# Kernel optimization log

Hardware: AMD Instinct MI355X
Metric: run time of the kernel (lower is better)

Reference implementation:

```python
import jax, jax.numpy as jnp
import numpy as np

B, L, C = 4, 2048, 512
H, D = 8, 512          # n_head, hidden_dim (per-head dim)
TEMP = 1.0
EPS = 1e-5


def setup_inputs() -> dict:
    key = jax.random.key(0)
    ks = jax.random.split(key, 12)
    s_in = 1.0 / np.sqrt(C)
    s_out = 1.0 / np.sqrt(H * D)
    return {
        "q": jax.random.normal(ks[0], (B, L, C), jnp.float32),
        "k": jax.random.normal(ks[1], (B, L, C), jnp.float32),
        "v": jax.random.normal(ks[2], (B, L, C), jnp.float32),
        "mask": jax.random.randint(ks[3], (B, L, L), 0, 2).astype(bool),
        "Wq": jax.random.normal(ks[4], (C, H * D), jnp.float32) * s_in,
        "bq": jnp.zeros((H * D,), jnp.float32),
        "Wk": jax.random.normal(ks[5], (C, H * D), jnp.float32) * s_in,
        "bk": jnp.zeros((H * D,), jnp.float32),
        "Wv": jax.random.normal(ks[6], (C, H * D), jnp.float32) * s_in,
        "bv": jnp.zeros((H * D,), jnp.float32),
        "Wo": jax.random.normal(ks[7], (H * D, D), jnp.float32) * s_out,
        "bo": jnp.zeros((D,), jnp.float32),
        "gamma": jnp.ones((D,), jnp.float32),
        "beta": jnp.zeros((D,), jnp.float32),
    }


def reference(q, k, v, mask, Wq, bq, Wk, bk, Wv, bv, Wo, bo, gamma, beta):
    b, ql, _ = q.shape
    residual = q
    qh = (q @ Wq + bq).reshape(b, ql, H, D)           # b,l,h,d
    kh = (k @ Wk + bk).reshape(b, ql, H, D)
    vh = (v @ Wv + bv).reshape(b, ql, H, D)
    # scores in head-major layout to mirror torch permute(2,0,1,3)
    scores = jnp.einsum("bqhd,bkhd->hbqk", qh, kh) / TEMP  # h,b,l,l
    scores = jnp.where(mask[None], -jnp.inf, scores)
    atten = jax.nn.softmax(scores, axis=-1)                 # h,b,l,l
    ctx = jnp.einsum("hbqk,bkhd->bqhd", atten, vh)          # b,l,h,d
    ctx = ctx.reshape(b, ql, H * D)
    out = ctx @ Wo + bo                                     # b,l,D  (dropout in eval mode)
    x = out + residual
    mu = jnp.mean(x, axis=-1, keepdims=True)
    var = jnp.var(x, axis=-1, keepdims=True)
    out = (x - mu) / jnp.sqrt(var + EPS) * gamma + beta
    return out, atten.reshape(H * b, ql, ql)
```

## Files before the change

kernel.cpp:

```cpp
#include <hip/hip_runtime.h>
#include <stdint.h>


typedef unsigned short u16;
typedef _Float16 f16;
typedef __attribute__((ext_vector_type(8))) _Float16 f16x8;
typedef __attribute__((ext_vector_type(4))) float f32x4;

#define OP_F16 0
#define OP_F32 1

#define EPI_QKH    0
#define EPI_VHT    1
#define EPI_SCORES 2
#define EPI_CTX    3
#define EPI_OUT    4

__device__ __forceinline__ f32x4 mfma16(f16x8 a, f16x8 b, f32x4 c) {
  return __builtin_amdgcn_mfma_f32_16x16x32_f16(a, b, c, 0, 0, 0);
}

__device__ __forceinline__ void stage_tile_f16(const char* gbase, size_t grow, char* lds, int tid) {
  const int lane = tid & 63, wave = tid >> 6;
#pragma unroll
  for (int c = 0; c < 2; ++c) {
    int chunk = wave * 2 + c;
    int off = chunk * 1024 + lane * 16;
    int r = off >> 6;
    int cb = off & 63;
    const char* g = gbase + (size_t)r * grow + cb;
    __builtin_amdgcn_global_load_lds(
        (__attribute__((address_space(1))) void*)g,
        (__attribute__((address_space(3))) void*)(lds + chunk * 1024),
        16, 0, 0);
  }
}

#define F32_ROWF 36
__device__ __forceinline__ void stage_tile_f32pad(const char* gbase, size_t grow, char* lds, int tid) {
#pragma unroll
  for (int c = 0; c < 4; ++c) {
    int idx = c * 256 + tid;
    int row = idx >> 3, col4 = idx & 7;
    f32x4 v = *(const f32x4*)(gbase + (size_t)row * grow + col4 * 16);
    *(f32x4*)(lds + (size_t)row * (F32_ROWF * 4) + col4 * 16) = v;
  }
}

template<int M>
__device__ __forceinline__ f16x8 load_frag(const char* lds, int row, int kq) {
  if constexpr (M == OP_F16) {
    return *(const f16x8*)(lds + ((size_t)row * 32 + kq) * 2);
  } else {
    size_t off = ((size_t)row * F32_ROWF + kq) * 4;
    f32x4 x0 = *(const f32x4*)(lds + off);
    f32x4 x1 = *(const f32x4*)(lds + off + 16);
    f16x8 h;
#pragma unroll
    for (int j = 0; j < 4; ++j) {
      h[j]     = (_Float16)x0[j];
      h[j + 4] = (_Float16)x1[j];
    }
    return h;
  }
}

template<int AM, int BM, int EPI>
__global__ __launch_bounds__(256, 2)
void gemm_k(const char* __restrict__ A, const char* __restrict__ B,
            int lda, int ldb, int K,
            char* __restrict__ C0,
            const float* __restrict__ bias, const float* __restrict__ resid) {
  constexpr int ASZ = (AM == OP_F16) ? 8192 : 128 * F32_ROWF * 4;
  constexpr int BSZ = (BM == OP_F16) ? 8192 : 128 * F32_ROWF * 4;
  __shared__ alignas(16) char smem[ASZ + BSZ];
  char* sA = smem;
  char* sB = smem + ASZ;

  const int tid = threadIdx.x, lane = tid & 63, wave = tid >> 6;
  const int wm = wave >> 1, wn = wave & 1;
  const int m0 = blockIdx.x * 128, n0 = blockIdx.y * 128;

  const char* pA = A; const char* pB = B;
  if constexpr (EPI == EPI_SCORES) {
    int z = blockIdx.z, h = z >> 2, b = z & 3;
    size_t e2 = ((size_t)b * 2048 * 4096 + (size_t)h * 512) * 2;
    pA += e2; pB += e2;
  } else if constexpr (EPI == EPI_CTX) {
    int z = blockIdx.z, h = z >> 2, b = z & 3;
    pA += ((size_t)z << 22) * 4;
    pB += ((size_t)(b * 8 + h) * 512 * 2048) * 2;
  }

  f32x4 acc[4][4];
#pragma unroll
  for (int i = 0; i < 4; ++i)
#pragma unroll
    for (int j = 0; j < 4; ++j) acc[i][j] = (f32x4){0.f, 0.f, 0.f, 0.f};

  for (int k0 = 0; k0 < K; k0 += 32) {
    if constexpr (AM == OP_F16)
      stage_tile_f16(pA + ((size_t)m0 * lda + k0) * 2, (size_t)lda * 2, sA, tid);
    else
      stage_tile_f32pad(pA + ((size_t)m0 * lda + k0) * 4, (size_t)lda * 4, sA, tid);
    if constexpr (BM == OP_F16)
      stage_tile_f16(pB + ((size_t)n0 * ldb + k0) * 2, (size_t)ldb * 2, sB, tid);
    else
      stage_tile_f32pad(pB + ((size_t)n0 * ldb + k0) * 4, (size_t)ldb * 4, sB, tid);
    __syncthreads();

    const int kq = (lane >> 4) * 8, l15 = lane & 15;
    f16x8 af[4], bf[4];
#pragma unroll
    for (int mi = 0; mi < 4; ++mi)
      af[mi] = load_frag<AM>(sA, wm * 64 + mi * 16 + l15, kq);
#pragma unroll
    for (int ni = 0; ni < 4; ++ni)
      bf[ni] = load_frag<BM>(sB, wn * 64 + ni * 16 + l15, kq);

#pragma unroll
    for (int mi = 0; mi < 4; ++mi)
#pragma unroll
      for (int ni = 0; ni < 4; ++ni)
        acc[mi][ni] = mfma16(af[mi], bf[ni], acc[mi][ni]);
    __syncthreads();
  }

  const int l15 = lane & 15, quad = lane >> 4;
#pragma unroll
  for (int mi = 0; mi < 4; ++mi)
#pragma unroll
    for (int ni = 0; ni < 4; ++ni)
#pragma unroll
      for (int r = 0; r < 4; ++r) {
        int m = m0 + wm * 64 + mi * 16 + quad * 4 + r;
        int n = n0 + wn * 64 + ni * 16 + l15;
        float v = acc[mi][ni][r];
        if constexpr (EPI == EPI_QKH) {
          v += bias[n];
          ((f16*)C0)[(size_t)m * 4096 + n] = (f16)v;
        } else if constexpr (EPI == EPI_VHT) {
          v += bias[m];
          int hh = m >> 9, d = m & 511, bb = n >> 11, ll = n & 2047;
          ((f16*)C0)[(((size_t)(bb * 8 + hh) * 512 + d) << 11) + ll] = (f16)v;
        } else if constexpr (EPI == EPI_SCORES) {
          int z = blockIdx.z;
          ((float*)C0)[((size_t)z << 22) + ((size_t)m << 11) + n] = v;
        } else if constexpr (EPI == EPI_CTX) {
          int z = blockIdx.z, hh = z >> 2, bb = z & 3;
          ((f16*)C0)[((size_t)(bb * 2048 + m) << 12) + hh * 512 + n] = (f16)v;
        } else {
          v += bias[n] + resid[((size_t)m << 9) + n];
          ((float*)C0)[((size_t)m << 9) + n] = v;
        }
      }
}

__global__ __launch_bounds__(256)
void transpose_cvt_k(const float* __restrict__ in, f16* __restrict__ T,
                     int rows_in, int cols_in) {
  int idx = blockIdx.x * 256 + threadIdx.x;
  if (idx >= rows_in * cols_in) return;
  int c = idx / rows_in, r = idx - c * rows_in;
  T[idx] = (f16)in[(size_t)r * cols_in + c];
}

__global__ __launch_bounds__(256)
void maskprep_k(const int* __restrict__ m32, unsigned char* __restrict__ m8) {
  int i = blockIdx.x * 256 + threadIdx.x;
  int4 v = ((const int4*)m32)[i];
  uchar4 c;
  c.x = (unsigned char)v.x; c.y = (unsigned char)v.y;
  c.z = (unsigned char)v.z; c.w = (unsigned char)v.w;
  ((uchar4*)m8)[i] = c;
}

__global__ __launch_bounds__(256)
void softmax_k(float* __restrict__ att, const unsigned char* __restrict__ m8) {
  __shared__ float sm[4];
  int t = threadIdx.x, lane = t & 63, wave = t >> 6;
  size_t r = blockIdx.x;
  int z = (int)(r >> 11), m = (int)(r & 2047), b = z & 3;
  float4* row = (float4*)(att + (r << 11));
  const uchar4* mrow = (const uchar4*)(m8 + (((size_t)b << 22) + ((size_t)m << 11)));
  float4 a = row[t], c = row[t + 256];
  uchar4 ma = mrow[t], mc = mrow[t + 256];
  if (ma.x) a.x = -1e30f; if (ma.y) a.y = -1e30f;
  if (ma.z) a.z = -1e30f; if (ma.w) a.w = -1e30f;
  if (mc.x) c.x = -1e30f; if (mc.y) c.y = -1e30f;
  if (mc.z) c.z = -1e30f; if (mc.w) c.w = -1e30f;
  float mx = fmaxf(fmaxf(fmaxf(a.x, a.y), fmaxf(a.z, a.w)),
                   fmaxf(fmaxf(c.x, c.y), fmaxf(c.z, c.w)));
#pragma unroll
  for (int o = 32; o > 0; o >>= 1) mx = fmaxf(mx, __shfl_xor(mx, o));
  if (lane == 0) sm[wave] = mx;
  __syncthreads();
  mx = fmaxf(fmaxf(sm[0], sm[1]), fmaxf(sm[2], sm[3]));
  a.x = __expf(a.x - mx); a.y = __expf(a.y - mx);
  a.z = __expf(a.z - mx); a.w = __expf(a.w - mx);
  c.x = __expf(c.x - mx); c.y = __expf(c.y - mx);
  c.z = __expf(c.z - mx); c.w = __expf(c.w - mx);
  float s = a.x + a.y + a.z + a.w + c.x + c.y + c.z + c.w;
#pragma unroll
  for (int o = 32; o > 0; o >>= 1) s += __shfl_xor(s, o);
  __syncthreads();
  if (lane == 0) sm[wave] = s;
  __syncthreads();
  s = sm[0] + sm[1] + sm[2] + sm[3];
  float inv = 1.0f / s;
  a.x *= inv; a.y *= inv; a.z *= inv; a.w *= inv;
  c.x *= inv; c.y *= inv; c.z *= inv; c.w *= inv;
  row[t] = a; row[t + 256] = c;
}

__global__ __launch_bounds__(256)
void ln_k(const float* __restrict__ x, const float* __restrict__ gamma,
          const float* __restrict__ beta, float* __restrict__ out) {
  __shared__ float s1[4], s2[4];
  int t = threadIdx.x, lane = t & 63, wave = t >> 6;
  size_t base = (size_t)blockIdx.x << 9;
  float2 v = ((const float2*)(x + base))[t];
  float s = v.x + v.y;
  float q = v.x * v.x + v.y * v.y;
#pragma unroll
  for (int o = 32; o > 0; o >>= 1) { s += __shfl_xor(s, o); q += __shfl_xor(q, o); }
  if (lane == 0) { s1[wave] = s; s2[wave] = q; }
  __syncthreads();
  s = s1[0] + s1[1] + s1[2] + s1[3];
  q = s2[0] + s2[1] + s2[2] + s2[3];
  float mu = s * (1.0f / 512.0f);
  float var = q * (1.0f / 512.0f) - mu * mu;
  float rs = rsqrtf(var + 1e-5f);
  float2 g = ((const float2*)gamma)[t];
  float2 bb = ((const float2*)beta)[t];
  float2 o2;
  o2.x = (v.x - mu) * rs * g.x + bb.x;
  o2.y = (v.y - mu) * rs * g.y + bb.y;
  ((float2*)(out + base))[t] = o2;
}

extern "C" void kernel_launch(void* const* d_in, const int* in_sizes, int n_in,
                              void* d_out, int out_size, void* d_ws, size_t ws_size,
                              hipStream_t stream) {
  (void)in_sizes; (void)n_in; (void)out_size; (void)ws_size;
  const float* q     = (const float*)d_in[0];
  const float* k     = (const float*)d_in[1];
  const float* v     = (const float*)d_in[2];
  const int*   mask  = (const int*)d_in[3];
  const float* Wq    = (const float*)d_in[4];
  const float* bq    = (const float*)d_in[5];
  const float* Wk    = (const float*)d_in[6];
  const float* bk    = (const float*)d_in[7];
  const float* Wv    = (const float*)d_in[8];
  const float* bv    = (const float*)d_in[9];
  const float* Wo    = (const float*)d_in[10];
  const float* bo    = (const float*)d_in[11];
  const float* gamma = (const float*)d_in[12];
  const float* beta  = (const float*)d_in[13];

  float* out0  = (float*)d_out;
  float* atten = out0 + (size_t)4 * 2048 * 512;

  char* ws = (char*)d_ws;
  const size_t MB = 1024ull * 1024ull;
  f16* WqT  = (f16*)(ws + 0 * MB);
  f16* WkT  = (f16*)(ws + 4 * MB);
  f16* WvT  = (f16*)(ws + 8 * MB);
  f16* WoT  = (f16*)(ws + 12 * MB);
  unsigned char* mask8 = (unsigned char*)(ws + 16 * MB);
  f16* vhT  = (f16*)(ws + 32 * MB);
  f16* qh   = (f16*)(ws + 96 * MB);
  f16* kh   = (f16*)(ws + 160 * MB);
  f16* ctx  = (f16*)(ws + 224 * MB);
  float* xbuf = (float*)(ws + 96 * MB);

  transpose_cvt_k<<<8192, 256, 0, stream>>>(Wq, WqT, 512, 4096);
  transpose_cvt_k<<<8192, 256, 0, stream>>>(Wk, WkT, 512, 4096);
  transpose_cvt_k<<<8192, 256, 0, stream>>>(Wv, WvT, 512, 4096);
  transpose_cvt_k<<<8192, 256, 0, stream>>>(Wo, WoT, 4096, 512);
  maskprep_k<<<16384, 256, 0, stream>>>(mask, mask8);

  gemm_k<OP_F32, OP_F16, EPI_QKH><<<dim3(64, 32, 1), 256, 0, stream>>>(
      (const char*)q, (const char*)WqT, 512, 512, 512, (char*)qh, bq, nullptr);
  gemm_k<OP_F32, OP_F16, EPI_QKH><<<dim3(64, 32, 1), 256, 0, stream>>>(
      (const char*)k, (const char*)WkT, 512, 512, 512, (char*)kh, bk, nullptr);

  gemm_k<OP_F16, OP_F32, EPI_VHT><<<dim3(32, 64, 1), 256, 0, stream>>>(
      (const char*)WvT, (const char*)v, 512, 512, 512, (char*)vhT, bv, nullptr);

  gemm_k<OP_F16, OP_F16, EPI_SCORES><<<dim3(16, 16, 32), 256, 0, stream>>>(
      (const char*)qh, (const char*)kh, 4096, 4096, 512, (char*)atten, nullptr, nullptr);

  softmax_k<<<65536, 256, 0, stream>>>(atten, mask8);

  gemm_k<OP_F32, OP_F16, EPI_CTX><<<dim3(16, 4, 32), 256, 0, stream>>>(
      (const char*)atten, (const char*)vhT, 2048, 2048, 2048, (char*)ctx, nullptr, nullptr);

  gemm_k<OP_F16, OP_F16, EPI_OUT><<<dim3(64, 4, 1), 256, 0, stream>>>(
      (const char*)ctx, (const char*)WoT, 4096, 4096, 4096, (char*)xbuf, bo, q);

  ln_k<<<8192, 256, 0, stream>>>(xbuf, gamma, beta, out0);
}
```

Baseline: 1.642 ms.

## Pre-convert GEMM operands to f16 so every GEMM uses async LDS staging

Adds a float-to-f16 conversion pass for q, k and v. Softmax now also writes an f16 copy of the attention matrix. The GEMM kernel keeps only the f16 path with direct global-to-LDS loads, which removes the register-staged padded f32 tiles and the per-fragment conversion in the inner loop. The context GEMM reads a half-size attention matrix, at the cost of an extra 256 MB write in softmax and three small conversion kernels. Workspace buffers are remapped so the f16 attention copy aliases buffers that are dead by the time softmax runs.

```diff
diff --git a/kernel.cpp b/kernel.cpp
--- a/kernel.cpp
+++ b/kernel.cpp
@@ -4,11 +4,9 @@
 
 typedef unsigned short u16;
 typedef _Float16 f16;
+typedef __attribute__((ext_vector_type(4))) _Float16 f16x4;
 typedef __attribute__((ext_vector_type(8))) _Float16 f16x8;
 typedef __attribute__((ext_vector_type(4))) float f32x4;
-
-#define OP_F16 0
-#define OP_F32 1
 
 #define EPI_QKH    0
 #define EPI_VHT    1
@@ -36,46 +34,19 @@
   }
 }
 
-#define F32_ROWF 36
-__device__ __forceinline__ void stage_tile_f32pad(const char* gbase, size_t grow, char* lds, int tid) {
-#pragma unroll
-  for (int c = 0; c < 4; ++c) {
-    int idx = c * 256 + tid;
-    int row = idx >> 3, col4 = idx & 7;
-    f32x4 v = *(const f32x4*)(gbase + (size_t)row * grow + col4 * 16);
-    *(f32x4*)(lds + (size_t)row * (F32_ROWF * 4) + col4 * 16) = v;
-  }
-}
-
-template<int M>
-__device__ __forceinline__ f16x8 load_frag(const char* lds, int row, int kq) {
-  if constexpr (M == OP_F16) {
-    return *(const f16x8*)(lds + ((size_t)row * 32 + kq) * 2);
-  } else {
-    size_t off = ((size_t)row * F32_ROWF + kq) * 4;
-    f32x4 x0 = *(const f32x4*)(lds + off);
-    f32x4 x1 = *(const f32x4*)(lds + off + 16);
-    f16x8 h;
-#pragma unroll
-    for (int j = 0; j < 4; ++j) {
-      h[j]     = (_Float16)x0[j];
-      h[j + 4] = (_Float16)x1[j];
-    }
-    return h;
-  }
-}
-
-template<int AM, int BM, int EPI>
+__device__ __forceinline__ f16x8 load_frag16(const char* lds, int row, int kq) {
+  return *(const f16x8*)(lds + ((size_t)row * 32 + kq) * 2);
+}
+
+template<int EPI>
 __global__ __launch_bounds__(256, 2)
 void gemm_k(const char* __restrict__ A, const char* __restrict__ B,
             int lda, int ldb, int K,
             char* __restrict__ C0,
             const float* __restrict__ bias, const float* __restrict__ resid) {
-  constexpr int ASZ = (AM == OP_F16) ? 8192 : 128 * F32_ROWF * 4;
-  constexpr int BSZ = (BM == OP_F16) ? 8192 : 128 * F32_ROWF * 4;
-  __shared__ alignas(16) char smem[ASZ + BSZ];
+  __shared__ alignas(16) char smem[16384];
   char* sA = smem;
-  char* sB = smem + ASZ;
+  char* sB = smem + 8192;
 
   const int tid = threadIdx.x, lane = tid & 63, wave = tid >> 6;
   const int wm = wave >> 1, wn = wave & 1;
@@ -88,7 +59,7 @@
     pA += e2; pB += e2;
   } else if constexpr (EPI == EPI_CTX) {
     int z = blockIdx.z, h = z >> 2, b = z & 3;
-    pA += ((size_t)z << 22) * 4;
+    pA += ((size_t)z << 22) * 2;
     pB += ((size_t)(b * 8 + h) * 512 * 2048) * 2;
   }
 
@@ -99,24 +70,18 @@
     for (int j = 0; j < 4; ++j) acc[i][j] = (f32x4){0.f, 0.f, 0.f, 0.f};
 
   for (int k0 = 0; k0 < K; k0 += 32) {
-    if constexpr (AM == OP_F16)
-      stage_tile_f16(pA + ((size_t)m0 * lda + k0) * 2, (size_t)lda * 2, sA, tid);
-    else
-      stage_tile_f32pad(pA + ((size_t)m0 * lda + k0) * 4, (size_t)lda * 4, sA, tid);
-    if constexpr (BM == OP_F16)
-      stage_tile_f16(pB + ((size_t)n0 * ldb + k0) * 2, (size_t)ldb * 2, sB, tid);
-    else
-      stage_tile_f32pad(pB + ((size_t)n0 * ldb + k0) * 4, (size_t)ldb * 4, sB, tid);
+    stage_tile_f16(pA + ((size_t)m0 * lda + k0) * 2, (size_t)lda * 2, sA, tid);
+    stage_tile_f16(pB + ((size_t)n0 * ldb + k0) * 2, (size_t)ldb * 2, sB, tid);
     __syncthreads();
 
     const int kq = (lane >> 4) * 8, l15 = lane & 15;
     f16x8 af[4], bf[4];
 #pragma unroll
     for (int mi = 0; mi < 4; ++mi)
-      af[mi] = load_frag<AM>(sA, wm * 64 + mi * 16 + l15, kq);
+      af[mi] = load_frag16(sA, wm * 64 + mi * 16 + l15, kq);
 #pragma unroll
     for (int ni = 0; ni < 4; ++ni)
-      bf[ni] = load_frag<BM>(sB, wn * 64 + ni * 16 + l15, kq);
+      bf[ni] = load_frag16(sB, wn * 64 + ni * 16 + l15, kq);
 
 #pragma unroll
     for (int mi = 0; mi < 4; ++mi)
@@ -166,6 +131,15 @@
 }
 
 __global__ __launch_bounds__(256)
+void cvt_f16_k(const float* __restrict__ in, f16* __restrict__ out) {
+  int i = blockIdx.x * 256 + threadIdx.x;
+  float4 v = ((const float4*)in)[i];
+  f16x4 h;
+  h[0] = (f16)v.x; h[1] = (f16)v.y; h[2] = (f16)v.z; h[3] = (f16)v.w;
+  ((f16x4*)out)[i] = h;
+}
+
+__global__ __launch_bounds__(256)
 void maskprep_k(const int* __restrict__ m32, unsigned char* __restrict__ m8) {
   int i = blockIdx.x * 256 + threadIdx.x;
   int4 v = ((const int4*)m32)[i];
@@ -176,7 +150,8 @@
 }
 
 __global__ __launch_bounds__(256)
-void softmax_k(float* __restrict__ att, const unsigned char* __restrict__ m8) {
+void softmax_k(float* __restrict__ att, const unsigned char* __restrict__ m8,
+               f16* __restrict__ att16) {
   __shared__ float sm[4];
   int t = threadIdx.x, lane = t & 63, wave = t >> 6;
   size_t r = blockIdx.x;
@@ -211,6 +186,11 @@
   a.x *= inv; a.y *= inv; a.z *= inv; a.w *= inv;
   c.x *= inv; c.y *= inv; c.z *= inv; c.w *= inv;
   row[t] = a; row[t + 256] = c;
+  f16x4* r16 = (f16x4*)(att16 + (r << 11));
+  f16x4 ha, hc;
+  ha[0] = (f16)a.x; ha[1] = (f16)a.y; ha[2] = (f16)a.z; ha[3] = (f16)a.w;
+  hc[0] = (f16)c.x; hc[1] = (f16)c.y; hc[2] = (f16)c.z; hc[3] = (f16)c.w;
+  r16[t] = ha; r16[t + 256] = hc;
 }
 
 __global__ __launch_bounds__(256)
@@ -268,35 +248,42 @@
   f16* WvT  = (f16*)(ws + 8 * MB);
   f16* WoT  = (f16*)(ws + 12 * MB);
   unsigned char* mask8 = (unsigned char*)(ws + 16 * MB);
-  f16* vhT  = (f16*)(ws + 32 * MB);
-  f16* qh   = (f16*)(ws + 96 * MB);
-  f16* kh   = (f16*)(ws + 160 * MB);
-  f16* ctx  = (f16*)(ws + 224 * MB);
-  float* xbuf = (float*)(ws + 96 * MB);
+  f16* q16  = (f16*)(ws + 32 * MB);
+  f16* k16  = (f16*)(ws + 40 * MB);
+  f16* v16  = (f16*)(ws + 48 * MB);
+  f16* vhT  = (f16*)(ws + 56 * MB);
+  f16* atten16 = (f16*)(ws + 120 * MB);
+  f16* qh   = (f16*)(ws + 120 * MB);
+  f16* kh   = (f16*)(ws + 184 * MB);
+  f16* ctx  = (f16*)(ws + 376 * MB);
+  float* xbuf = (float*)(ws + 120 * MB);
 
   transpose_cvt_k<<<8192, 256, 0, stream>>>(Wq, WqT, 512, 4096);
   transpose_cvt_k<<<8192, 256, 0, stream>>>(Wk, WkT, 512, 4096);
   transpose_cvt_k<<<8192, 256, 0, stream>>>(Wv, WvT, 512, 4096);
   transpose_cvt_k<<<8192, 256, 0, stream>>>(Wo, WoT, 4096, 512);
   maskprep_k<<<16384, 256, 0, stream>>>(mask, mask8);
-
-  gemm_k<OP_F32, OP_F16, EPI_QKH><<<dim3(64, 32, 1), 256, 0, stream>>>(
-      (const char*)q, (const char*)WqT, 512, 512, 512, (char*)qh, bq, nullptr);
-  gemm_k<OP_F32, OP_F16, EPI_QKH><<<dim3(64, 32, 1), 256, 0, stream>>>(
-      (const char*)k, (const char*)WkT, 512, 512, 512, (char*)kh, bk, nullptr);
-
-  gemm_k<OP_F16, OP_F32, EPI_VHT><<<dim3(32, 64, 1), 256, 0, stream>>>(
-      (const char*)WvT, (const char*)v, 512, 512, 512, (char*)vhT, bv, nullptr);
-
-  gemm_k<OP_F16, OP_F16, EPI_SCORES><<<dim3(16, 16, 32), 256, 0, stream>>>(
+  cvt_f16_k<<<4096, 256, 0, stream>>>(q, q16);
+  cvt_f16_k<<<4096, 256, 0, stream>>>(k, k16);
+  cvt_f16_k<<<4096, 256, 0, stream>>>(v, v16);
+
+  gemm_k<EPI_QKH><<<dim3(64, 32, 1), 256, 0, stream>>>(
+      (const char*)q16, (const char*)WqT, 512, 512, 512, (char*)qh, bq, nullptr);
+  gemm_k<EPI_QKH><<<dim3(64, 32, 1), 256, 0, stream>>>(
+      (const char*)k16, (const char*)WkT, 512, 512, 512, (char*)kh, bk, nullptr);
+
+  gemm_k<EPI_VHT><<<dim3(32, 64, 1), 256, 0, stream>>>(
+      (const char*)WvT, (const char*)v16, 512, 512, 512, (char*)vhT, bv, nullptr);
+
+  gemm_k<EPI_SCORES><<<dim3(16, 16, 32), 256, 0, stream>>>(
       (const char*)qh, (const char*)kh, 4096, 4096, 512, (char*)atten, nullptr, nullptr);
 
-  softmax_k<<<65536, 256, 0, stream>>>(atten, mask8);
-
-  gemm_k<OP_F32, OP_F16, EPI_CTX><<<dim3(16, 4, 32), 256, 0, stream>>>(
-      (const char*)atten, (const char*)vhT, 2048, 2048, 2048, (char*)ctx, nullptr, nullptr);
-
-  gemm_k<OP_F16, OP_F16, EPI_OUT><<<dim3(64, 4, 1), 256, 0, stream>>>(
+  softmax_k<<<65536, 256, 0, stream>>>(atten, mask8, atten16);
+
+  gemm_k<EPI_CTX><<<dim3(16, 4, 32), 256, 0, stream>>>(
+      (const char*)atten16, (const char*)vhT, 2048, 2048, 2048, (char*)ctx, nullptr, nullptr);
+
+  gemm_k<EPI_OUT><<<dim3(64, 4, 1), 256, 0, stream>>>(
       (const char*)ctx, (const char*)WoT, 4096, 4096, 4096, (char*)xbuf, bo, q);
 
   ln_k<<<8192, 256, 0, stream>>>(xbuf, gamma, beta, out0);
```

New measurement: 1.588 ms. -3.3%, faster.
